# Kernel tuning notes

Hardware: AMD Instinct MI355X
Metric: run time of the kernel (lower is better)

The kernel has to match this reference:

```python
import jax, jax.numpy as jnp
import numpy as np

N = 100000      # nodes
E = 1600000     # edges (before self-loops)
D_IN = 128      # node_attr_size
H = 4           # gat_heads
C = 32          # hidden_size (per-head out channels)
F = H * C       # feature_size = 128
K = 16          # num_clusters
L = 2           # num_gat_layers
EPS = 1e-5
NEG_SLOPE = 0.2  # PyG GATv2Conv default leaky_relu slope


def setup_inputs() -> dict:
    key = jax.random.key(0)
    ks = jax.random.split(key, 8)
    x = jax.random.normal(ks[0], (N, D_IN), jnp.float32)
    edge_index = jax.random.randint(ks[1], (2, E), 0, N, jnp.int32)
    sF = 1.0 / np.sqrt(F).astype(np.float32)
    Wp = jax.random.normal(ks[2], (D_IN, F), jnp.float32) * (1.0 / np.sqrt(D_IN).astype(np.float32))
    bp = jnp.zeros((F,), jnp.float32)
    ln_g = jnp.ones((L, F), jnp.float32)
    ln_b = jnp.zeros((L, F), jnp.float32)
    Wl = jax.random.normal(ks[3], (L, F, H * C), jnp.float32) * sF
    bl = jnp.zeros((L, H * C), jnp.float32)
    Wr = jax.random.normal(ks[4], (L, F, H * C), jnp.float32) * sF
    br = jnp.zeros((L, H * C), jnp.float32)
    att = jax.random.normal(ks[5], (L, H, C), jnp.float32) * (1.0 / np.sqrt(C).astype(np.float32))
    gb = jnp.zeros((L, F), jnp.float32)  # GATv2Conv output bias
    Wc = jax.random.normal(ks[6], (F, K), jnp.float32) * sF
    bc = jnp.zeros((K,), jnp.float32)
    return dict(x=x, edge_index=edge_index, Wp=Wp, bp=bp, ln_g=ln_g, ln_b=ln_b,
                Wl=Wl, bl=bl, Wr=Wr, br=br, att=att, gb=gb, Wc=Wc, bc=bc)


def _layernorm(x, g, b):
    mu = jnp.mean(x, axis=-1, keepdims=True)
    var = jnp.var(x, axis=-1, keepdims=True)
    return (x - mu) * jax.lax.rsqrt(var + EPS) * g + b


def reference(x, edge_index, Wp, bp, ln_g, ln_b, Wl, bl, Wr, br, att, gb, Wc, bc):
    # GATv2Conv adds self-loops by default
    loops = jnp.arange(N, dtype=edge_index.dtype)
    src = jnp.concatenate([edge_index[0], loops])  # message source j
    dst = jnp.concatenate([edge_index[1], loops])  # message target i

    h = x @ Wp + bp  # node_feat_proj -> [N, F]
    for i in range(L):
        identity = h
        hn = _layernorm(h, ln_g[i], ln_b[i])
        x_l = (hn @ Wl[i] + bl[i]).reshape(N, H, C)  # source transform
        x_r = (hn @ Wr[i] + br[i]).reshape(N, H, C)  # target transform
        m = x_l[src] + x_r[dst]                       # [E+N, H, C]
        s = jnp.where(m > 0, m, NEG_SLOPE * m)        # leaky_relu(0.2)
        logits = jnp.einsum('ehc,hc->eh', s, att[i])  # [E+N, H]
        # segment softmax over incoming edges of each target node
        mx = jax.ops.segment_max(logits, dst, num_segments=N)
        a = jnp.exp(logits - mx[dst])
        den = jax.ops.segment_sum(a, dst, num_segments=N)
        alpha = a / den[dst]
        out = jax.ops.segment_sum(x_l[src] * alpha[:, :, None], dst, num_segments=N)
        out = out.reshape(N, F) + gb[i]
        # relu activation, dropout identity (eval), residual add
        h = jax.nn.relu(out) + identity

    classification_output = h @ Wc + bc
    return (classification_output, h)
```

## Files before the change

### kernel.cpp

```cpp
#include <hip/hip_runtime.h>
#include <hip/hip_bf16.h>
#include <math.h>
#include <stdint.h>

#define N_NODES 100000
#define N_EDGES 1600000
#define ET (N_EDGES + N_NODES)
#define FDIM 128
#define NK 16
#define EPS 1e-5f
#define SLOPE 0.2f

typedef __attribute__((ext_vector_type(8))) short bf16x8;
typedef __attribute__((ext_vector_type(4))) float f32x4;
typedef __attribute__((ext_vector_type(2))) _Float16 h2;

__device__ inline unsigned pk_bf16(float a, float b) {
    float2 f; f.x = a; f.y = b;
    __hip_bfloat162 t = __float22bfloat162_rn(f);
    return *reinterpret_cast<unsigned*>(&t);
}
__device__ inline h2 as_h2(unsigned u) { return __builtin_bit_cast(h2, u); }
__device__ inline unsigned as_u(h2 v) { return __builtin_bit_cast(unsigned, v); }

#define DPPF(X, CTRL) __int_as_float(__builtin_amdgcn_mov_dpp(__float_as_int(X), (CTRL), 0xF, 0xF, true))
#define DX1(X) DPPF(X, 0xB1)
#define DX2(X) DPPF(X, 0x4E)
#define DR4(X) DPPF(X, 0x124)
#define DR8(X) DPPF(X, 0x128)
#define DB0(X) DPPF(X, 0x00)
#define DB1(X) DPPF(X, 0x55)
#define DB2(X) DPPF(X, 0xAA)
#define DB3(X) DPPF(X, 0xFF)

__device__ inline float exp2_hw(float x) {
    float r;
    asm("v_exp_f32 %0, %1" : "=v"(r) : "v"(x));
    return r;
}

#define FMAMIX_LO(ACC, U, W) \
    asm("v_fma_mix_f32 %0, %1, %2, %0 op_sel_hi:[1,0,0]" : "+v"(ACC) : "v"(U), "v"(W))
#define FMAMIX_HI(ACC, U, W) \
    asm("v_fma_mix_f32 %0, %1, %2, %0 op_sel:[1,0,0] op_sel_hi:[1,0,0]" : "+v"(ACC) : "v"(U), "v"(W))

__device__ inline int rflm(int v) { return __builtin_amdgcn_readfirstlane(v) & 131071; }


#define NBKT 196
#define BSH 9
#define BSTRIDE 10240
#define P1_EPT 8
#define P1_EPB (256 * P1_EPT)
#define PART_BLOCKS ((ET + P1_EPB - 1) / P1_EPB)

__global__ __launch_bounds__(256) void prep_kernel(
        const int* __restrict__ ei, int* __restrict__ gcount,
        int* __restrict__ staging,
        const float* __restrict__ Wp, const float* __restrict__ Wl,
        const float* __restrict__ Wr, ushort* __restrict__ wbp,
        ushort* __restrict__ wbl0, ushort* __restrict__ wbl1) {
    __shared__ int hist[NBKT];
    __shared__ int lofs[NBKT];
    __shared__ int gbase[NBKT];
    __shared__ int s[256];
    __shared__ int spk[P1_EPB];
    __shared__ short sbk[P1_EPB];
    int bid = blockIdx.x;
    int t = threadIdx.x;
    if (bid >= PART_BLOCKS) {
        int bb = bid - PART_BLOCKS;
        const float *W0, *W1; ushort* out; int nt;
        if (bb < 8)       { W0 = Wp; W1 = Wp; out = wbp; nt = bb; }
        else if (bb < 24) { W0 = Wl; W1 = Wr; out = wbl0; nt = bb - 8; }
        else              { W0 = Wl + FDIM * FDIM; W1 = Wr + FDIM * FDIM; out = wbl1; nt = bb - 24; }
        int kk = t >> 6, lane = t & 63;
        int n = nt * 16 + (lane & 15);
        int k0 = kk * 32 + (lane >> 4) * 8;
        const float* W = (n < 128) ? (W0 + n) : (W1 + (n - 128));
        float f[8];
#pragma unroll
        for (int j = 0; j < 8; j++) f[j] = W[(size_t)(k0 + j) * FDIM];
        uint4 u;
        u.x = pk_bf16(f[0], f[1]); u.y = pk_bf16(f[2], f[3]);
        u.z = pk_bf16(f[4], f[5]); u.w = pk_bf16(f[6], f[7]);
        *(uint4*)&out[(size_t)((nt * 4 + kk) * 64 + lane) * 8] = u;
        return;
    }
    if (t < NBKT) hist[t] = 0;
    __syncthreads();
    int e0 = bid * P1_EPB + t;
    int pk[P1_EPT], bk[P1_EPT], rk[P1_EPT];
#pragma unroll
    for (int k = 0; k < P1_EPT; k++) {
        int e = e0 + k * 256;
        bk[k] = -1;
        if (e < ET) {
            int src, dst;
            if (e < N_EDGES) { src = ei[e]; dst = ei[N_EDGES + e]; }
            else             { src = dst = e - N_EDGES; }
            int b = dst >> BSH;
            pk[k] = (src << BSH) | (dst & 511);
            bk[k] = b;
            rk[k] = atomicAdd(&hist[b], 1);
        }
    }
    __syncthreads();
    int v = (t < NBKT) ? hist[t] : 0;
    s[t] = v;
    __syncthreads();
    for (int o = 1; o < 256; o <<= 1) {
        int add = (t >= o) ? s[t - o] : 0;
        __syncthreads();
        s[t] += add;
        __syncthreads();
    }
    if (t < NBKT) {
        lofs[t] = s[t] - v;
        gbase[t] = (v > 0) ? atomicAdd(&gcount[t], v) : 0;
    }
    __syncthreads();
#pragma unroll
    for (int k = 0; k < P1_EPT; k++) {
        if (bk[k] >= 0) {
            int idx = lofs[bk[k]] + rk[k];
            spk[idx] = pk[k];
            sbk[idx] = (short)bk[k];
        }
    }
    __syncthreads();
    int tot = lofs[NBKT - 1] + hist[NBKT - 1];
    for (int i = t; i < tot; i += 256) {
        int b = sbk[i];
        staging[b * BSTRIDE + gbase[b] + (i - lofs[b])] = spk[i];
    }
}

__global__ __launch_bounds__(256) void csr_proj_kernel(
        const int* __restrict__ staging, const int* __restrict__ gcount,
        int* __restrict__ off, int* __restrict__ perm,
        const float* __restrict__ x, const ushort* __restrict__ wb,
        const float* __restrict__ bp, float* __restrict__ h) {
    __shared__ uint4 fragbuf[4 * 272];
    int bid = blockIdx.x;
    int t = threadIdx.x;
    if (bid >= NBKT) {
        int wid = ((bid - NBKT) * 256 + t) >> 6;
        int lane = t & 63;
        if (wid >= N_NODES / 16) return;
        uint4* fb = fragbuf + (t >> 6) * 272;
        int q = lane >> 4, m = lane & 15;
        int row0 = wid * 16;
        const float* xrow = x + (size_t)(row0 + m) * FDIM + q * 32;
#pragma unroll
        for (int p = 0; p < 4; p++) {
            float4 a = *(const float4*)&xrow[p * 8];
            float4 c = *(const float4*)&xrow[p * 8 + 4];
            uint4 u;
            u.x = pk_bf16(a.x, a.y); u.y = pk_bf16(a.z, a.w);
            u.z = pk_bf16(c.x, c.y); u.w = pk_bf16(c.z, c.w);
            fb[q * 68 + p * 17 + m] = u;
        }
        bf16x8 A[4];
#pragma unroll
        for (int kk = 0; kk < 4; kk++)
            A[kk] = *(const bf16x8*)&fb[kk * 68 + q * 17 + m];
        const bf16x8* wbv = (const bf16x8*)wb;
        f32x4 acc[8];
        f32x4 z = {0.f, 0.f, 0.f, 0.f};
#pragma unroll
        for (int nt = 0; nt < 8; nt++) acc[nt] = z;
#pragma unroll
        for (int nt = 0; nt < 8; nt++) {
#pragma unroll
            for (int kk = 0; kk < 4; kk++) {
                bf16x8 B = wbv[(nt * 4 + kk) * 64 + lane];
                acc[nt] = __builtin_amdgcn_mfma_f32_16x16x32_bf16(A[kk], B, acc[nt], 0, 0, 0);
            }
        }
#pragma unroll
        for (int nt = 0; nt < 8; nt++) {
            int col = nt * 16 + m;
            float bias = bp[col];
#pragma unroll
            for (int r = 0; r < 4; r++)
                h[(size_t)(row0 + q * 4 + r) * FDIM + col] = acc[nt][r] + bias;
        }
        return;
    }
    int* hist = (int*)fragbuf;
    int* cur  = hist + 512;
    int* pr   = cur + 512;
    int* gpre = pr + 256;
    int b = bid;
    hist[t] = 0; hist[t + 256] = 0;
    gpre[t] = (t < NBKT) ? gcount[t] : 0;
    __syncthreads();
    int sz = gcount[b];
    for (int k = t; k < sz; k += 256)
        atomicAdd(&hist[staging[b * BSTRIDE + k] & 511], 1);
    __syncthreads();
    int a0 = hist[2 * t], a1 = hist[2 * t + 1];
    pr[t] = a0 + a1;
    __syncthreads();
    for (int o = 1; o < 256; o <<= 1) {
        int ad = (t >= o) ? pr[t - o] : 0;
        int gd = (t >= o) ? gpre[t - o] : 0;
        __syncthreads();
        pr[t] += ad;
        gpre[t] += gd;
        __syncthreads();
    }
    int base = gpre[b] - sz;
    int pe = pr[t] - (a0 + a1);
    cur[2 * t] = pe;
    cur[2 * t + 1] = pe + a0;
    int n = (b << BSH) + 2 * t;
    if (n < N_NODES)     off[n]     = base + pe;
    if (n + 1 < N_NODES) off[n + 1] = base + pe + a0;
    if (b == 0 && t == 0) off[N_NODES] = ET;
    __syncthreads();
    for (int k = t; k < sz; k += 256) {
        int p = staging[b * BSTRIDE + k];
        int slot = atomicAdd(&cur[p & 511], 1);
        perm[base + slot] = p >> BSH;
    }
}


__global__ __launch_bounds__(256) void ln_gemm2_kernel(
        const float* __restrict__ h,
        const float* __restrict__ g, const float* __restrict__ b,
        const ushort* __restrict__ wb, const float* __restrict__ bl,
        const float* __restrict__ br,
        ushort* __restrict__ xlh, ushort* __restrict__ xrh) {
    __shared__ uint4 fragbuf[4 * 272];
    int wid = (blockIdx.x * 256 + threadIdx.x) >> 6;
    int lane = threadIdx.x & 63;
    if (wid >= N_NODES / 16) return;
    uint4* fb = fragbuf + (threadIdx.x >> 6) * 272;
    int q = lane >> 4, m = lane & 15;
    int row0 = wid * 16;
    const float* hrow = h + (size_t)(row0 + m) * FDIM + q * 32;
    float v[32];
#pragma unroll
    for (int i = 0; i < 8; i++) {
        float4 t4 = *(const float4*)&hrow[i * 4];
        v[i * 4 + 0] = t4.x; v[i * 4 + 1] = t4.y; v[i * 4 + 2] = t4.z; v[i * 4 + 3] = t4.w;
    }
    float s = 0.f, ss = 0.f;
#pragma unroll
    for (int i = 0; i < 32; i++) { s += v[i]; ss += v[i] * v[i]; }
    s  += __shfl_xor(s, 16);  s  += __shfl_xor(s, 32);
    ss += __shfl_xor(ss, 16); ss += __shfl_xor(ss, 32);
    float mu = s * (1.f / 128.f);
    float var = ss * (1.f / 128.f) - mu * mu;
    float rv = rsqrtf(var + EPS);
#pragma unroll
    for (int i = 0; i < 8; i++) {
        float4 gv = *(const float4*)&g[q * 32 + i * 4];
        float4 bv = *(const float4*)&b[q * 32 + i * 4];
        v[i * 4 + 0] = (v[i * 4 + 0] - mu) * rv * gv.x + bv.x;
        v[i * 4 + 1] = (v[i * 4 + 1] - mu) * rv * gv.y + bv.y;
        v[i * 4 + 2] = (v[i * 4 + 2] - mu) * rv * gv.z + bv.z;
        v[i * 4 + 3] = (v[i * 4 + 3] - mu) * rv * gv.w + bv.w;
    }
#pragma unroll
    for (int p = 0; p < 4; p++) {
        uint4 u;
        u.x = pk_bf16(v[p * 8 + 0], v[p * 8 + 1]);
        u.y = pk_bf16(v[p * 8 + 2], v[p * 8 + 3]);
        u.z = pk_bf16(v[p * 8 + 4], v[p * 8 + 5]);
        u.w = pk_bf16(v[p * 8 + 6], v[p * 8 + 7]);
        fb[q * 68 + p * 17 + m] = u;
    }
    bf16x8 A[4];
#pragma unroll
    for (int kk = 0; kk < 4; kk++)
        A[kk] = *(const bf16x8*)&fb[kk * 68 + q * 17 + m];
    const bf16x8* wbv = (const bf16x8*)wb;
    f32x4 acc[16];
    f32x4 z = {0.f, 0.f, 0.f, 0.f};
#pragma unroll
    for (int nt = 0; nt < 16; nt++) acc[nt] = z;
#pragma unroll
    for (int nt = 0; nt < 16; nt++) {
#pragma unroll
        for (int kk = 0; kk < 4; kk++) {
            bf16x8 B = wbv[(nt * 4 + kk) * 64 + lane];
            acc[nt] = __builtin_amdgcn_mfma_f32_16x16x32_bf16(A[kk], B, acc[nt], 0, 0, 0);
        }
    }
#pragma unroll
    for (int nt = 0; nt < 16; nt++) {
        int col = nt * 16 + m;
        if (nt < 8) {
            float bias = bl[col];
#pragma unroll
            for (int r = 0; r < 4; r++) {
                _Float16 hf = (_Float16)(acc[nt][r] + bias);
                xlh[(size_t)(row0 + q * 4 + r) * FDIM + col] = __builtin_bit_cast(ushort, hf);
            }
        } else {
            int c2 = col - 128;
            float bias = br[c2];
#pragma unroll
            for (int r = 0; r < 4; r++) {
                _Float16 hf = (_Float16)(acc[nt][r] + bias);
                xrh[(size_t)(row0 + q * 4 + r) * FDIM + c2] = __builtin_bit_cast(ushort, hf);
            }
        }
    }
}

__global__ __launch_bounds__(256) void final_kernel(const float* __restrict__ h,
                                                    const float* __restrict__ Wc,
                                                    const float* __restrict__ bc,
                                                    float* __restrict__ out) {
    __shared__ float sh[16][128];
    int row0 = blockIdx.x * 16;
    int t = threadIdx.x;
    for (int i = t; i < 512; i += 256) {
        int r = i >> 5, c4 = (i & 31) * 4;
        *(float4*)&sh[r][c4] = *(const float4*)&h[(size_t)(row0 + r) * FDIM + c4];
    }
    __syncthreads();
    int m = t >> 4, k = t & 15;
    float acc = 0.f;
    for (int c = 0; c < 128; c += 4) {
        const float4 xv = *(const float4*)&sh[m][c];
        acc += xv.x * Wc[(c + 0) * NK + k] + xv.y * Wc[(c + 1) * NK + k]
             + xv.z * Wc[(c + 2) * NK + k] + xv.w * Wc[(c + 3) * NK + k];
    }
    out[(size_t)(row0 + m) * NK + k] = acc + bc[k];
}


__global__ __launch_bounds__(256) void gat_agg_kernel(
        const unsigned* __restrict__ xlp, const unsigned* __restrict__ xrp,
        const int* __restrict__ off, const int* __restrict__ perm,
        const float* __restrict__ att, const float* __restrict__ gb,
        float* __restrict__ h) {
    int wave = (blockIdx.x * 256 + threadIdx.x) >> 6;
    unsigned lane = threadIdx.x & 63;
    int iA = wave * 2;
    if (iA >= N_NODES) return;
    int iB = iA + 1;
    int2 oA = *(const int2*)&off[iA];
    int eB2 = off[iB + 1];
    h2 xrvA = as_h2(xrp[(unsigned)iA * 64u + lane]);
    h2 xrvB = as_h2(xrp[(unsigned)iB * 64u + lane]);
    const float2 hidA = *(const float2*)&h[(size_t)iA * FDIM + lane * 2];
    const float2 hidB = *(const float2*)&h[(size_t)iB * FDIM + lane * 2];
    const float2 gbv = *(const float2*)&gb[lane * 2];
    float2 attf = *(const float2*)&att[lane * 2];
    h2 attp; attp[0] = (_Float16)(attf.x * 1.44269504f);
    attp[1] = (_Float16)(attf.y * 1.44269504f);
    const h2 c06 = {(_Float16)0.6f, (_Float16)0.6f};
    const h2 c04 = {(_Float16)0.4f, (_Float16)0.4f};
    bool b0 = lane & 1, b1 = lane & 2;
    int begA = __builtin_amdgcn_readfirstlane(oA.x);
    int endA = __builtin_amdgcn_readfirstlane(oA.y);
    int begB = endA;
    int endB = __builtin_amdgcn_readfirstlane(eB2);
    const char* xlB_ = (const char*)xlp;
    unsigned laneB = lane << 2;

#define GLD(J) (*(const unsigned*)(xlB_ + ((unsigned)(J) * 256u + laneB)))

#define EDGE_PARTIAL(XRV, U, T)                                     \
    {                                                               \
        h2 mm = as_h2(U) + XRV;                                     \
        h2 am = as_h2(as_u(mm) & 0x7FFF7FFFu);                      \
        h2 sv = am * c04 + mm * c06;                                \
        T = __builtin_amdgcn_fdot2(sv, attp, 0.f, false);           \
    }

#define COMPUTE4(S, U0, U1, U2, U3)                                 \
    {                                                               \
        float t0, t1, t2, t3;                                       \
        EDGE_PARTIAL(xrv##S, U0, t0);                               \
        EDGE_PARTIAL(xrv##S, U1, t1);                               \
        EDGE_PARTIAL(xrv##S, U2, t2);                               \
        EDGE_PARTIAL(xrv##S, U3, t3);                               \
        float u   = b0 ? t1 : t0;                                   \
        float uu2 = b0 ? t0 : t1;                                   \
        u += DX1(uu2);                                              \
        float vv  = b0 ? t3 : t2;                                   \
        float vv2 = b0 ? t2 : t3;                                   \
        vv += DX1(vv2);                                             \
        float ww  = b1 ? vv : u;                                    \
        float ww2 = b1 ? u : vv;                                    \
        ww += DX2(ww2);                                             \
        ww += DR4(ww);                                              \
        ww += DR8(ww);                                              \
        float ew = exp2_hw(ww);                                     \
        dloc##S += ew;                                              \
        float w0 = DB0(ew);                                         \
        float w1 = DB1(ew);                                         \
        float w2 = DB2(ew);                                         \
        float w3 = DB3(ew);                                         \
        FMAMIX_LO(accx##S, U0, w0); FMAMIX_HI(accy##S, U0, w0);     \
        FMAMIX_LO(accx##S, U1, w1); FMAMIX_HI(accy##S, U1, w1);     \
        FMAMIX_LO(accx##S, U2, w2); FMAMIX_HI(accy##S, U2, w2);     \
        FMAMIX_LO(accx##S, U3, w3); FMAMIX_HI(accy##S, U3, w3);     \
    }

#define TAIL1(S, U)                                                 \
    {                                                               \
        float tt;                                                   \
        EDGE_PARTIAL(xrv##S, U, tt);                                \
        tt += DX1(tt);                                              \
        tt += DX2(tt);                                              \
        tt += DR4(tt);                                              \
        tt += DR8(tt);                                              \
        float w = exp2_hw(tt);                                      \
        if ((lane & 3) == 0) dloc##S += w;                          \
        FMAMIX_LO(accx##S, U, w); FMAMIX_HI(accy##S, U, w);         \
    }

    int nbA = (endA - begA) >> 2, tlA = (endA - begA) & 3;
    int nbB = (endB - begB) >> 2, tlB = (endB - begB) & 3;
    float accxA = 0.f, accyA = 0.f, dlocA = 0.f;
    float accxB = 0.f, accyB = 0.f, dlocB = 0.f;
    unsigned c0A, c1A, c2A, c3A, d0A, d1A, d2A, d3A; int4 p2A;
    unsigned c0B, c1B, c2B, c3B, d0B, d1B, d2B, d3B; int4 p2B;
    unsigned t0A = 0, t1A = 0, t2A = 0, t0B = 0, t1B = 0, t2B = 0;
    int4 p0A, p1A, ptA, p0B, p1B, ptB;

    if (nbA > 0) {
        __builtin_memcpy(&p0A, perm + begA, 16);
        __builtin_memcpy(&p1A, perm + begA + 4, 16);
        __builtin_memcpy(&p2A, perm + begA + 8, 16);
    }
    if (tlA > 0) __builtin_memcpy(&ptA, perm + begA + 4 * nbA, 16);
    if (nbB > 0) {
        __builtin_memcpy(&p0B, perm + begB, 16);
        __builtin_memcpy(&p1B, perm + begB + 4, 16);
        __builtin_memcpy(&p2B, perm + begB + 8, 16);
    }
    if (tlB > 0) __builtin_memcpy(&ptB, perm + begB + 4 * nbB, 16);
    if (nbA > 0) {
        c0A = GLD(rflm(p0A.x)); c1A = GLD(rflm(p0A.y)); c2A = GLD(rflm(p0A.z)); c3A = GLD(rflm(p0A.w));
        d0A = GLD(rflm(p1A.x)); d1A = GLD(rflm(p1A.y)); d2A = GLD(rflm(p1A.z)); d3A = GLD(rflm(p1A.w));
    }
    if (nbB > 0) {
        c0B = GLD(rflm(p0B.x)); c1B = GLD(rflm(p0B.y)); c2B = GLD(rflm(p0B.z)); c3B = GLD(rflm(p0B.w));
        d0B = GLD(rflm(p1B.x)); d1B = GLD(rflm(p1B.y)); d2B = GLD(rflm(p1B.z)); d3B = GLD(rflm(p1B.w));
    }
    if (tlA > 0) {
        t0A = GLD(rflm(ptA.x));
        if (tlA > 1) t1A = GLD(rflm(ptA.y));
        if (tlA > 2) t2A = GLD(rflm(ptA.z));
    }
    if (tlB > 0) {
        t0B = GLD(rflm(ptB.x));
        if (tlB > 1) t1B = GLD(rflm(ptB.y));
        if (tlB > 2) t2B = GLD(rflm(ptB.z));
    }

    int blkA = 0, blkB = 0;
    while (blkA + 2 < nbA && blkB + 2 < nbB) {
        unsigned e0 = GLD(rflm(p2A.x)), e1 = GLD(rflm(p2A.y));
        unsigned e2 = GLD(rflm(p2A.z)), e3 = GLD(rflm(p2A.w));
        unsigned f0 = GLD(rflm(p2B.x)), f1 = GLD(rflm(p2B.y));
        unsigned f2 = GLD(rflm(p2B.z)), f3 = GLD(rflm(p2B.w));
        __builtin_memcpy(&p2A, perm + begA + 4 * blkA + 12, 16);
        __builtin_memcpy(&p2B, perm + begB + 4 * blkB + 12, 16);
        COMPUTE4(A, c0A, c1A, c2A, c3A);
        c0A = d0A; c1A = d1A; c2A = d2A; c3A = d3A;
        d0A = e0; d1A = e1; d2A = e2; d3A = e3;
        COMPUTE4(B, c0B, c1B, c2B, c3B);
        c0B = d0B; c1B = d1B; c2B = d2B; c3B = d3B;
        d0B = f0; d1B = f1; d2B = f2; d3B = f3;
        ++blkA; ++blkB;
    }
    for (; blkA + 2 < nbA; ++blkA) {
        unsigned e0 = GLD(rflm(p2A.x)), e1 = GLD(rflm(p2A.y));
        unsigned e2 = GLD(rflm(p2A.z)), e3 = GLD(rflm(p2A.w));
        __builtin_memcpy(&p2A, perm + begA + 4 * blkA + 12, 16);
        COMPUTE4(A, c0A, c1A, c2A, c3A);
        c0A = d0A; c1A = d1A; c2A = d2A; c3A = d3A;
        d0A = e0; d1A = e1; d2A = e2; d3A = e3;
    }
    for (; blkB + 2 < nbB; ++blkB) {
        unsigned f0 = GLD(rflm(p2B.x)), f1 = GLD(rflm(p2B.y));
        unsigned f2 = GLD(rflm(p2B.z)), f3 = GLD(rflm(p2B.w));
        __builtin_memcpy(&p2B, perm + begB + 4 * blkB + 12, 16);
        COMPUTE4(B, c0B, c1B, c2B, c3B);
        c0B = d0B; c1B = d1B; c2B = d2B; c3B = d3B;
        d0B = f0; d1B = f1; d2B = f2; d3B = f3;
    }
    if (nbA >= 2) {
        COMPUTE4(A, c0A, c1A, c2A, c3A);
        c0A = d0A; c1A = d1A; c2A = d2A; c3A = d3A;
    }
    if (nbB >= 2) {
        COMPUTE4(B, c0B, c1B, c2B, c3B);
        c0B = d0B; c1B = d1B; c2B = d2B; c3B = d3B;
    }
    if (nbA >= 1) COMPUTE4(A, c0A, c1A, c2A, c3A);
    if (nbB >= 1) COMPUTE4(B, c0B, c1B, c2B, c3B);
    if (tlA > 0) {
        TAIL1(A, t0A);
        if (tlA > 1) TAIL1(A, t1A);
        if (tlA > 2) TAIL1(A, t2A);
    }
    if (tlB > 0) {
        TAIL1(B, t0B);
        if (tlB > 1) TAIL1(B, t1B);
        if (tlB > 2) TAIL1(B, t2B);
    }
#undef EDGE_PARTIAL
#undef COMPUTE4
#undef TAIL1
#undef GLD

    float denA = dlocA + DX1(dlocA);
    denA += DX2(denA);
    float invA = 1.f / denA;
    float2 resA;
    resA.x = fmaxf(accxA * invA + gbv.x, 0.f) + hidA.x;
    resA.y = fmaxf(accyA * invA + gbv.y, 0.f) + hidA.y;
    *(float2*)&h[(size_t)iA * FDIM + lane * 2] = resA;
    float denB = dlocB + DX1(dlocB);
    denB += DX2(denB);
    float invB = 1.f / denB;
    float2 resB;
    resB.x = fmaxf(accxB * invB + gbv.x, 0.f) + hidB.x;
    resB.y = fmaxf(accyB * invB + gbv.y, 0.f) + hidB.y;
    *(float2*)&h[(size_t)iB * FDIM + lane * 2] = resB;
}


extern "C" void kernel_launch(void* const* d_in, const int* in_sizes, int n_in,
                              void* d_out, int out_size, void* d_ws, size_t ws_size,
                              hipStream_t stream) {
    const float* x    = (const float*)d_in[0];
    const int*   ei   = (const int*)  d_in[1];
    const float* Wp   = (const float*)d_in[2];
    const float* bp   = (const float*)d_in[3];
    const float* ln_g = (const float*)d_in[4];
    const float* ln_b = (const float*)d_in[5];
    const float* Wl   = (const float*)d_in[6];
    const float* bl   = (const float*)d_in[7];
    const float* Wr   = (const float*)d_in[8];
    const float* br   = (const float*)d_in[9];
    const float* att  = (const float*)d_in[10];
    const float* gb   = (const float*)d_in[11];
    const float* Wc   = (const float*)d_in[12];
    const float* bc   = (const float*)d_in[13];

    float* out_cls = (float*)d_out;
    float* h = out_cls + (size_t)N_NODES * NK;

    char* w = (char*)d_ws;
    int* off    = (int*)w; w += (size_t)(N_NODES + 1) * sizeof(int);
    int* gcount = (int*)w; w += 256 * sizeof(int);
    int* perm   = (int*)w; w += (size_t)ET * sizeof(int);
    uintptr_t a = ((uintptr_t)w + 255) & ~(uintptr_t)255;
    ushort* xlh = (ushort*)a;
    ushort* xrh = xlh + (size_t)N_NODES * FDIM;
    ushort* wbp = xrh + (size_t)N_NODES * FDIM;
    ushort* wbl0 = wbp + 8 * 4 * 64 * 8;
    ushort* wbl1 = wbl0 + 16 * 4 * 64 * 8;
    int* staging = (int*)xlh;

    hipMemsetAsync(gcount, 0, NBKT * sizeof(int), stream);
    prep_kernel<<<PART_BLOCKS + 40, 256, 0, stream>>>(
        ei, gcount, staging, Wp, Wl, Wr, wbp, wbl0, wbl1);
    csr_proj_kernel<<<NBKT + (N_NODES / 16 + 3) / 4, 256, 0, stream>>>(
        staging, gcount, off, perm, x, wbp, bp, h);

    const int gw = (N_NODES / 16 + 3) / 4;
    for (int l = 0; l < 2; ++l) {
        ln_gemm2_kernel<<<gw, 256, 0, stream>>>(
            h, ln_g + l * FDIM, ln_b + l * FDIM,
            (l == 0) ? wbl0 : wbl1, bl + l * FDIM, br + l * FDIM,
            xlh, xrh);
        gat_agg_kernel<<<(N_NODES / 2) / 4, 256, 0, stream>>>(
            (const unsigned*)xlh, (const unsigned*)xrh, off, perm,
            att + l * FDIM, gb + l * FDIM, h);
    }

    final_kernel<<<N_NODES / 16, 256, 0, stream>>>(h, Wc, bc, out_cls);
}
```

Baseline: 445.0 us.

## Fuse first LN+GEMM into projection kernel and classifier into last aggregation

The node projection kernel now also runs layer-0 layernorm and the Wl/Wr GEMM on its register tile, provided the workspace has room for a separate staging buffer so xlh/xrh are not aliased. The final classifier GEMM is folded into the second GAT aggregation kernel, which stages Wc in shared memory and writes the class logits directly. This removes two kernel launches and the re-reading of h from global memory, at the cost of more registers and LDS in the fused kernels. It also removes the early-return bounds guard in the aggregation kernel.

Measured after the change: 391.7 us. 1.14x faster.

```diff
diff --git a/kernel.cpp b/kernel.cpp
--- a/kernel.cpp
+++ b/kernel.cpp
@@ -23,6 +23,7 @@
 __device__ inline h2 as_h2(unsigned u) { return __builtin_bit_cast(h2, u); }
 __device__ inline unsigned as_u(h2 v) { return __builtin_bit_cast(unsigned, v); }
 
+#define SWZ(X, P) __int_as_float(__builtin_amdgcn_ds_swizzle(__float_as_int(X), (P)))
 #define DPPF(X, CTRL) __int_as_float(__builtin_amdgcn_mov_dpp(__float_as_int(X), (CTRL), 0xF, 0xF, true))
 #define DX1(X) DPPF(X, 0xB1)
 #define DX2(X) DPPF(X, 0x4E)
@@ -136,11 +137,15 @@
     }
 }
 
-__global__ __launch_bounds__(256) void csr_proj_kernel(
+__global__ __launch_bounds__(256) void csr_projln_kernel(
         const int* __restrict__ staging, const int* __restrict__ gcount,
         int* __restrict__ off, int* __restrict__ perm,
         const float* __restrict__ x, const ushort* __restrict__ wb,
-        const float* __restrict__ bp, float* __restrict__ h) {
+        const float* __restrict__ bp, float* __restrict__ h,
+        const ushort* __restrict__ wbl,
+        const float* __restrict__ g_, const float* __restrict__ b_,
+        const float* __restrict__ bl, const float* __restrict__ br,
+        ushort* __restrict__ xlh, ushort* __restrict__ xrh) {
     __shared__ uint4 fragbuf[4 * 272];
     int bid = blockIdx.x;
     int t = threadIdx.x;
@@ -178,13 +183,73 @@
                 acc[nt] = __builtin_amdgcn_mfma_f32_16x16x32_bf16(A[kk], B, acc[nt], 0, 0, 0);
             }
         }
+        float hv[8][4];
 #pragma unroll
         for (int nt = 0; nt < 8; nt++) {
             int col = nt * 16 + m;
             float bias = bp[col];
 #pragma unroll
-            for (int r = 0; r < 4; r++)
-                h[(size_t)(row0 + q * 4 + r) * FDIM + col] = acc[nt][r] + bias;
+            for (int r = 0; r < 4; r++) {
+                hv[nt][r] = acc[nt][r] + bias;
+                h[(size_t)(row0 + q * 4 + r) * FDIM + col] = hv[nt][r];
+            }
+        }
+        if (!wbl) return;
+        float gc[8], bcv[8];
+#pragma unroll
+        for (int nt = 0; nt < 8; nt++) { gc[nt] = g_[nt * 16 + m]; bcv[nt] = b_[nt * 16 + m]; }
+        ushort* fbu = (ushort*)fb;
+#pragma unroll
+        for (int r = 0; r < 4; r++) {
+            float s = 0.f, ss = 0.f;
+#pragma unroll
+            for (int nt = 0; nt < 8; nt++) { s += hv[nt][r]; ss += hv[nt][r] * hv[nt][r]; }
+            s += SWZ(s, 0x041F); s += SWZ(s, 0x081F); s += SWZ(s, 0x101F); s += SWZ(s, 0x201F);
+            ss += SWZ(ss, 0x041F); ss += SWZ(ss, 0x081F); ss += SWZ(ss, 0x101F); ss += SWZ(ss, 0x201F);
+            float mu = s * (1.f / 128.f);
+            float rv = rsqrtf(ss * (1.f / 128.f) - mu * mu + EPS);
+#pragma unroll
+            for (int nt = 0; nt < 8; nt++) {
+                float val = (hv[nt][r] - mu) * rv * gc[nt] + bcv[nt];
+                ushort us = (ushort)pk_bf16(val, val);
+                fbu[(((nt >> 1) * 68 + ((nt & 1) * 2 + (m >> 3)) * 17 + (q * 4 + r)) << 3) + (m & 7)] = us;
+            }
+        }
+        bf16x8 A2[4];
+#pragma unroll
+        for (int kk = 0; kk < 4; kk++)
+            A2[kk] = *(const bf16x8*)&fb[kk * 68 + q * 17 + m];
+        const bf16x8* wlv = (const bf16x8*)wbl;
+        f32x4 acc2[16];
+#pragma unroll
+        for (int nt = 0; nt < 16; nt++) acc2[nt] = z;
+#pragma unroll
+        for (int nt = 0; nt < 16; nt++) {
+#pragma unroll
+            for (int kk = 0; kk < 4; kk++) {
+                bf16x8 B = wlv[(nt * 4 + kk) * 64 + lane];
+                acc2[nt] = __builtin_amdgcn_mfma_f32_16x16x32_bf16(A2[kk], B, acc2[nt], 0, 0, 0);
+            }
+        }
+#pragma unroll
+        for (int nt = 0; nt < 16; nt++) {
+            int col = nt * 16 + m;
+            if (nt < 8) {
+                float bias = bl[col];
+#pragma unroll
+                for (int r = 0; r < 4; r++) {
+                    _Float16 hf = (_Float16)(acc2[nt][r] + bias);
+                    xlh[(size_t)(row0 + q * 4 + r) * FDIM + col] = __builtin_bit_cast(ushort, hf);
+                }
+            } else {
+                int c2 = col - 128;
+                float bias = br[c2];
+#pragma unroll
+                for (int r = 0; r < 4; r++) {
+                    _Float16 hf = (_Float16)(acc2[nt][r] + bias);
+                    xrh[(size_t)(row0 + q * 4 + r) * FDIM + c2] = __builtin_bit_cast(ushort, hf);
+                }
+            }
         }
         return;
     }
@@ -313,38 +378,24 @@
     }
 }
 
-__global__ __launch_bounds__(256) void final_kernel(const float* __restrict__ h,
-                                                    const float* __restrict__ Wc,
-                                                    const float* __restrict__ bc,
-                                                    float* __restrict__ out) {
-    __shared__ float sh[16][128];
-    int row0 = blockIdx.x * 16;
-    int t = threadIdx.x;
-    for (int i = t; i < 512; i += 256) {
-        int r = i >> 5, c4 = (i & 31) * 4;
-        *(float4*)&sh[r][c4] = *(const float4*)&h[(size_t)(row0 + r) * FDIM + c4];
-    }
-    __syncthreads();
-    int m = t >> 4, k = t & 15;
-    float acc = 0.f;
-    for (int c = 0; c < 128; c += 4) {
-        const float4 xv = *(const float4*)&sh[m][c];
-        acc += xv.x * Wc[(c + 0) * NK + k] + xv.y * Wc[(c + 1) * NK + k]
-             + xv.z * Wc[(c + 2) * NK + k] + xv.w * Wc[(c + 3) * NK + k];
-    }
-    out[(size_t)(row0 + m) * NK + k] = acc + bc[k];
-}
-
 
 __global__ __launch_bounds__(256) void gat_agg_kernel(
         const unsigned* __restrict__ xlp, const unsigned* __restrict__ xrp,
         const int* __restrict__ off, const int* __restrict__ perm,
         const float* __restrict__ att, const float* __restrict__ gb,
-        float* __restrict__ h) {
+        float* __restrict__ h,
+        const float* __restrict__ Wc, const float* __restrict__ bc,
+        float* __restrict__ out_cls) {
+    __shared__ float WcS[FDIM * NK];
+    __shared__ float hbuf[4 * 256];
+    bool dofinal = (Wc != nullptr);
+    if (dofinal) {
+        for (int i = threadIdx.x; i < FDIM * NK; i += 256) WcS[i] = Wc[i];
+        __syncthreads();
+    }
     int wave = (blockIdx.x * 256 + threadIdx.x) >> 6;
     unsigned lane = threadIdx.x & 63;
     int iA = wave * 2;
-    if (iA >= N_NODES) return;
     int iB = iA + 1;
     int2 oA = *(const int2*)&off[iA];
     int eB2 = off[iB + 1];
@@ -530,6 +581,29 @@
     resB.x = fmaxf(accxB * invB + gbv.x, 0.f) + hidB.x;
     resB.y = fmaxf(accyB * invB + gbv.y, 0.f) + hidB.y;
     *(float2*)&h[(size_t)iB * FDIM + lane * 2] = resB;
+
+    if (dofinal) {
+        float* sh = hbuf + (threadIdx.x >> 6) * 256;
+        sh[lane * 2]       = resA.x; sh[lane * 2 + 1]       = resA.y;
+        sh[128 + lane * 2] = resB.x; sh[128 + lane * 2 + 1] = resB.y;
+        int k = lane & 15, g = lane >> 4;
+        float pA = 0.f, pB = 0.f;
+#pragma unroll 8
+        for (int c = g * 32; c < g * 32 + 32; ++c) {
+            float wv = WcS[c * NK + k];
+            pA = fmaf(sh[c], wv, pA);
+            pB = fmaf(sh[128 + c], wv, pB);
+        }
+        pA += SWZ(pA, 0x401F);
+        pB += SWZ(pB, 0x401F);
+        pA += __shfl_xor(pA, 32);
+        pB += __shfl_xor(pB, 32);
+        if (g == 0) {
+            float bk = bc[k];
+            out_cls[(size_t)iA * NK + k] = pA + bk;
+            out_cls[(size_t)iB * NK + k] = pB + bk;
+        }
+    }
 }
 
 
@@ -564,24 +638,29 @@
     ushort* wbp = xrh + (size_t)N_NODES * FDIM;
     ushort* wbl0 = wbp + 8 * 4 * 64 * 8;
     ushort* wbl1 = wbl0 + 16 * 4 * 64 * 8;
-    int* staging = (int*)xlh;
+    char* wend = (char*)(wbl1 + 16 * 4 * 64 * 8);
+    size_t need = (size_t)(wend - (char*)d_ws) + (size_t)NBKT * BSTRIDE * sizeof(int);
+    bool roomy = (ws_size >= need);
+    int* staging = roomy ? (int*)wend : (int*)xlh;
 
     hipMemsetAsync(gcount, 0, NBKT * sizeof(int), stream);
     prep_kernel<<<PART_BLOCKS + 40, 256, 0, stream>>>(
         ei, gcount, staging, Wp, Wl, Wr, wbp, wbl0, wbl1);
-    csr_proj_kernel<<<NBKT + (N_NODES / 16 + 3) / 4, 256, 0, stream>>>(
-        staging, gcount, off, perm, x, wbp, bp, h);
-
     const int gw = (N_NODES / 16 + 3) / 4;
-    for (int l = 0; l < 2; ++l) {
+    csr_projln_kernel<<<NBKT + gw, 256, 0, stream>>>(
+        staging, gcount, off, perm, x, wbp, bp, h,
+        roomy ? wbl0 : (const ushort*)nullptr,
+        ln_g, ln_b, bl, br, xlh, xrh);
+    if (!roomy)
         ln_gemm2_kernel<<<gw, 256, 0, stream>>>(
-            h, ln_g + l * FDIM, ln_b + l * FDIM,
-            (l == 0) ? wbl0 : wbl1, bl + l * FDIM, br + l * FDIM,
-            xlh, xrh);
-        gat_agg_kernel<<<(N_NODES / 2) / 4, 256, 0, stream>>>(
-            (const unsigned*)xlh, (const unsigned*)xrh, off, perm,
-            att + l * FDIM, gb + l * FDIM, h);
-    }
-
-    final_kernel<<<N_NODES / 16, 256, 0, stream>>>(h, Wc, bc, out_cls);
+            h, ln_g, ln_b, wbl0, bl, br, xlh, xrh);
+
+    gat_agg_kernel<<<(N_NODES / 2) / 4, 256, 0, stream>>>(
+        (const unsigned*)xlh, (const unsigned*)xrh, off, perm,
+        att, gb, h, nullptr, nullptr, nullptr);
+    ln_gemm2_kernel<<<gw, 256, 0, stream>>>(
+        h, ln_g + FDIM, ln_b + FDIM, wbl1, bl + FDIM, br + FDIM, xlh, xrh);
+    gat_agg_kernel<<<(N_NODES / 2) / 4, 256, 0, stream>>>(
+        (const unsigned*)xlh, (const unsigned*)xrh, off, perm,
+        att + FDIM, gb + FDIM, h, Wc, bc, out_cls);
 }
```
